# Optimization experiments

Hardware: AMD Instinct MI355X
Metric: run time of the kernel (lower is better)

The kernel has to match this reference:

```python
import jax, jax.numpy as jnp
import numpy as np

EPS = 1e-06

def _feature_map(x):
    # elu(x) + 1 -> strictly positive feature map
    return jax.nn.elu(x) + 1.0

def setup_inputs() -> dict:
    key = jax.random.key(0)
    kq, kk, kv = jax.random.split(key, 3)
    B, H, N, D = 1, 16, 2048, 64
    Q = jax.random.normal(kq, (B, H, N, D), dtype=jnp.float32)
    K = jax.random.normal(kk, (B, H, N, D), dtype=jnp.float32)
    V = jax.random.normal(kv, (B, H, N, D), dtype=jnp.float32)
    return {"Q": Q, "K": K, "V": V, "causal": 1}

def reference(Q, K, V, causal):
    Qf = _feature_map(Q)  # (B,H,N,D)
    Kf = _feature_map(K)  # (B,H,N,D)
    if causal:
        # prefix sums of per-position outer products K_m V_m^T  -> (B,H,N,D,Dv)
        KV_prefix = jnp.cumsum(Kf[..., :, None] * V[..., None, :], axis=2)
        Kf_prefix = jnp.cumsum(Kf, axis=2)  # (B,H,N,D)
        num = jnp.einsum('bhnd,bhnde->bhne', Qf, KV_prefix)
        den = jnp.einsum('bhnd,bhnd->bhn', Qf, Kf_prefix)[..., None]
        return num / (den + EPS)
    else:
        KV = jnp.einsum('bhnd,bhne->bhde', Kf, V)            # (B,H,D,Dv)
        num = jnp.einsum('bhnd,bhde->bhne', Qf, KV)          # (B,H,N,Dv)
        den = jnp.einsum('bhnd,bhd->bhn', Qf, Kf.sum(axis=2))[..., None]
        return num / (den + EPS)
```

## Files before the change

kernel.cpp:

```cpp
#include <hip/hip_runtime.h>

#define Hh   16
#define Nn   2048
#define Dd   64
#define DVv  64
#define Ll   64
#define Cc   (Nn / Ll)
#define HCc  (Hh * Cc)
#define EPSf 1e-6f
#define LDP  72

typedef __attribute__((ext_vector_type(8))) __bf16 bf16x8;
typedef __attribute__((ext_vector_type(4))) __bf16 bf16x4;
typedef __attribute__((ext_vector_type(4))) float  f32x4;

__device__ __forceinline__ float fmap(float x) {
    return x > 0.0f ? (x + 1.0f) : __expf(x);
}
__device__ __forceinline__ __bf16 tobf(float x) { return (__bf16)x; }

__global__ __launch_bounds__(256) void k_chunk_sums(
    const float* __restrict__ Kg, const float* __restrict__ Vg,
    __bf16* __restrict__ SwsT, float* __restrict__ zws)
{
    __shared__ __align__(16) __bf16 sKT[Dd][LDP];
    __shared__ __align__(16) __bf16 sVT[80][LDP];
    const int t  = threadIdx.x;
    const int hc = blockIdx.x;
    const float4* K4 = (const float4*)(Kg + (size_t)hc * (Ll * Dd));
    const float4* V4 = (const float4*)(Vg + (size_t)hc * (Ll * DVv));
    for (int i = t; i < (Ll * Dd) / 4; i += 256) {
        float4 k4 = K4[i];
        float4 v4 = V4[i];
        const int m  = i >> 4;
        const int c0 = (i & 15) * 4;
        sKT[c0 + 0][m] = tobf(fmap(k4.x));
        sKT[c0 + 1][m] = tobf(fmap(k4.y));
        sKT[c0 + 2][m] = tobf(fmap(k4.z));
        sKT[c0 + 3][m] = tobf(fmap(k4.w));
        sVT[c0 + 0][m] = tobf(v4.x);
        sVT[c0 + 1][m] = tobf(v4.y);
        sVT[c0 + 2][m] = tobf(v4.z);
        sVT[c0 + 3][m] = tobf(v4.w);
    }
    for (int i = t; i < 16 * LDP; i += 256) {
        const int r = i / LDP, c = i % LDP;
        sVT[64 + r][c] = (r == 0) ? (__bf16)1.0f : (__bf16)0.0f;
    }
    __syncthreads();

    const int lane = t & 63, wv = t >> 6;
    const int col = lane & 15, quad = lane >> 4;
    __bf16* So = SwsT + (size_t)hc * (Dd * DVv);
    for (int et = 0; et < 5; ++et) {
        f32x4 acc = {0.f, 0.f, 0.f, 0.f};
#pragma unroll
        for (int ks = 0; ks < 2; ++ks) {
            bf16x8 a = *(const bf16x8*)&sKT[wv * 16 + col][ks * 32 + quad * 8];
            bf16x8 b = *(const bf16x8*)&sVT[et * 16 + col][ks * 32 + quad * 8];
            acc = __builtin_amdgcn_mfma_f32_16x16x32_bf16(a, b, acc, 0, 0, 0);
        }
        if (et < 4) {
            const int e = et * 16 + col;
            const int d = wv * 16 + quad * 4;
            bf16x4 s4 = { tobf(acc[0]), tobf(acc[1]), tobf(acc[2]), tobf(acc[3]) };
            *(bf16x4*)&So[e * Dd + d] = s4;
        } else if (col == 0) {
#pragma unroll
            for (int j = 0; j < 4; ++j)
                zws[hc * Dd + wv * 16 + quad * 4 + j] = acc[j];
        }
    }
}

__global__ __launch_bounds__(256) void k_prefix(
    __bf16* __restrict__ SwsT, float* __restrict__ zws)
{
    const int b = blockIdx.x, t = threadIdx.x;
    if (b < 32) {
        const int gid = b * 256 + t;
        const int h   = gid >> 9;
        const int sl  = gid & 511;
        __bf16* base = SwsT + ((size_t)h * Cc) * (Dd * DVv) + sl * 8;
        float run[8];
#pragma unroll
        for (int j = 0; j < 8; ++j) run[j] = 0.0f;
#pragma unroll
        for (int cb = 0; cb < 4; ++cb) {
            bf16x8 v[8];
#pragma unroll
            for (int k = 0; k < 8; ++k)
                v[k] = *(const bf16x8*)(base + (size_t)(cb * 8 + k) * (Dd * DVv));
#pragma unroll
            for (int k = 0; k < 8; ++k) {
                bf16x8 o;
#pragma unroll
                for (int j = 0; j < 8; ++j) {
                    o[j] = tobf(run[j]);
                    run[j] += (float)v[k][j];
                }
                *(bf16x8*)(base + (size_t)(cb * 8 + k) * (Dd * DVv)) = o;
            }
        }
    } else {
        const int gid = (b - 32) * 256 + t;
        const int h = gid >> 6, d = gid & 63;
        float* zb = zws + (h * Cc) * Dd + d;
        float run = 0.0f;
#pragma unroll
        for (int cb = 0; cb < 4; ++cb) {
            float v[8];
#pragma unroll
            for (int k = 0; k < 8; ++k) v[k] = zb[(cb * 8 + k) * Dd];
#pragma unroll
            for (int k = 0; k < 8; ++k) {
                zb[(cb * 8 + k) * Dd] = run;
                run += v[k];
            }
        }
    }
}

__global__ __launch_bounds__(256) void k_output(
    const float* __restrict__ Qg, const float* __restrict__ Kg,
    const float* __restrict__ Vg, const __bf16* __restrict__ SwsT,
    const float* __restrict__ zws, float* __restrict__ Og)
{
    __shared__ __align__(16) __bf16 aQ[Ll][LDP];
    __shared__ __align__(16) __bf16 aK[Ll][LDP];
    __shared__ __align__(16) __bf16 sW[Ll][LDP];
    __shared__ __align__(16) __bf16 bV[80][LDP];
    __shared__ __align__(16) __bf16 bS[80][LDP];
    const int t  = threadIdx.x;
    const int hc = blockIdx.x;
    const int lane = t & 63, wv = t >> 6;
    const int col = lane & 15, quad = lane >> 4;

    {
        const float4* Q4 = (const float4*)(Qg + (size_t)hc * (Ll * Dd));
        const float4* K4 = (const float4*)(Kg + (size_t)hc * (Ll * Dd));
        const float4* V4 = (const float4*)(Vg + (size_t)hc * (Ll * DVv));
        for (int i = t; i < (Ll * Dd) / 4; i += 256) {
            float4 q4 = Q4[i];
            float4 k4 = K4[i];
            float4 v4 = V4[i];
            const int m  = i >> 4;
            const int c0 = (i & 15) * 4;
            bf16x4 qv = { tobf(fmap(q4.x)), tobf(fmap(q4.y)), tobf(fmap(q4.z)), tobf(fmap(q4.w)) };
            bf16x4 kv = { tobf(fmap(k4.x)), tobf(fmap(k4.y)), tobf(fmap(k4.z)), tobf(fmap(k4.w)) };
            *(bf16x4*)&aQ[m][c0] = qv;
            *(bf16x4*)&aK[m][c0] = kv;
            bV[c0 + 0][m] = tobf(v4.x);
            bV[c0 + 1][m] = tobf(v4.y);
            bV[c0 + 2][m] = tobf(v4.z);
            bV[c0 + 3][m] = tobf(v4.w);
        }
        for (int i = t; i < 16 * LDP; i += 256) {
            const int r = i / LDP, cc = i % LDP;
            bV[64 + r][cc] = (r == 0) ? (__bf16)1.0f : (__bf16)0.0f;
        }
    }

    {
        const __bf16* Sp = SwsT + (size_t)hc * (Dd * DVv);
        for (int i = t; i < (Dd * DVv) / 8; i += 256) {
            bf16x8 s = *(const bf16x8*)(Sp + i * 8);
            const int e = i >> 3, d0 = (i & 7) * 8;
            *(bf16x8*)&bS[e][d0] = s;
        }
        if (t < Dd) bS[64][t] = tobf(zws[hc * Dd + t]);
        for (int i = t; i < 16 * LDP; i += 256) {
            const int r = i / LDP, cc = i % LDP;
            if (!(r == 0 && cc < Dd)) bS[64 + r][cc] = (__bf16)0.0f;
        }
    }
    __syncthreads();

#pragma unroll 1
    for (int mt = 0; mt < 4; ++mt) {
        f32x4 wacc = {0.f, 0.f, 0.f, 0.f};
#pragma unroll
        for (int ks = 0; ks < 2; ++ks) {
            bf16x8 a = *(const bf16x8*)&aQ[wv * 16 + col][ks * 32 + quad * 8];
            bf16x8 b = *(const bf16x8*)&aK[mt * 16 + col][ks * 32 + quad * 8];
            wacc = __builtin_amdgcn_mfma_f32_16x16x32_bf16(a, b, wacc, 0, 0, 0);
        }
#pragma unroll
        for (int j = 0; j < 4; ++j) {
            const int n = wv * 16 + quad * 4 + j;
            const int m = mt * 16 + col;
            sW[n][m] = tobf(m <= n ? wacc[j] : 0.0f);
        }
    }
    __syncthreads();

    f32x4 accs[5];
#pragma unroll 1
    for (int et = 0; et < 5; ++et) {
        f32x4 acc = {0.f, 0.f, 0.f, 0.f};
#pragma unroll
        for (int ks = 0; ks < 2; ++ks) {
            bf16x8 a = *(const bf16x8*)&sW[wv * 16 + col][ks * 32 + quad * 8];
            bf16x8 b = *(const bf16x8*)&bV[et * 16 + col][ks * 32 + quad * 8];
            acc = __builtin_amdgcn_mfma_f32_16x16x32_bf16(a, b, acc, 0, 0, 0);
        }
#pragma unroll
        for (int ks = 0; ks < 2; ++ks) {
            bf16x8 a = *(const bf16x8*)&aQ[wv * 16 + col][ks * 32 + quad * 8];
            bf16x8 b = *(const bf16x8*)&bS[et * 16 + col][ks * 32 + quad * 8];
            acc = __builtin_amdgcn_mfma_f32_16x16x32_bf16(a, b, acc, 0, 0, 0);
        }
        accs[et] = acc;
    }
    float dn[4];
#pragma unroll
    for (int j = 0; j < 4; ++j) dn[j] = __shfl(accs[4][j], lane & 48);

    float* Oc = Og + (size_t)hc * (Ll * DVv);
#pragma unroll
    for (int et = 0; et < 4; ++et) {
#pragma unroll
        for (int j = 0; j < 4; ++j) {
            const int n = wv * 16 + quad * 4 + j;
            Oc[n * DVv + et * 16 + col] = accs[et][j] / (dn[j] + EPSf);
        }
    }
}

extern "C" void kernel_launch(void* const* d_in, const int* in_sizes, int n_in,
                              void* d_out, int out_size, void* d_ws, size_t ws_size,
                              hipStream_t stream) {
    const float* Q = (const float*)d_in[0];
    const float* K = (const float*)d_in[1];
    const float* V = (const float*)d_in[2];
    __bf16* SwsT = (__bf16*)d_ws;
    float*  zws  = (float*)((char*)d_ws + (size_t)HCc * Dd * DVv * sizeof(__bf16));
    float* out = (float*)d_out;

    k_chunk_sums<<<HCc, 256, 0, stream>>>(K, V, SwsT, zws);
    k_prefix<<<36, 256, 0, stream>>>(SwsT, zws);
    k_output<<<HCc, 256, 0, stream>>>(Q, K, V, SwsT, zws, out);
}
```

Before: 88.78 us.

## Fuse chunk-sum and prefix-scan kernels via last-block-per-head atomic counter

Merges the separate prefix-scan kernel into the chunk-sum kernel. The last block to finish for each head, found through an atomic counter, performs that head's prefix scan over the chunk state matrices and normaliser sums. This removes one kernel launch and its inter-kernel gap. In exchange it adds a memset on the same stream, threadfences, and serialised scan work on 16 blocks that each handle a whole head, so per-thread scan work is larger than in the old 36-block scan.

New measurement: 160.7 us. +81.0%, slower.

```diff
diff --git a/kernel.cpp b/kernel.cpp
--- a/kernel.cpp
+++ b/kernel.cpp
@@ -19,14 +19,17 @@
 }
 __device__ __forceinline__ __bf16 tobf(float x) { return (__bf16)x; }
 
-__global__ __launch_bounds__(256) void k_chunk_sums(
+__global__ __launch_bounds__(256) void k_chunk_scan(
     const float* __restrict__ Kg, const float* __restrict__ Vg,
-    __bf16* __restrict__ SwsT, float* __restrict__ zws)
+    __bf16* __restrict__ SwsT, float* __restrict__ zws,
+    unsigned int* __restrict__ cnt)
 {
     __shared__ __align__(16) __bf16 sKT[Dd][LDP];
     __shared__ __align__(16) __bf16 sVT[80][LDP];
+    __shared__ int isLast;
     const int t  = threadIdx.x;
     const int hc = blockIdx.x;
+    const int h  = hc >> 5;
     const float4* K4 = (const float4*)(Kg + (size_t)hc * (Ll * Dd));
     const float4* V4 = (const float4*)(Vg + (size_t)hc * (Ll * DVv));
     for (int i = t; i < (Ll * Dd) / 4; i += 256) {
@@ -71,51 +74,51 @@
                 zws[hc * Dd + wv * 16 + quad * 4 + j] = acc[j];
         }
     }
-}
-
-__global__ __launch_bounds__(256) void k_prefix(
-    __bf16* __restrict__ SwsT, float* __restrict__ zws)
-{
-    const int b = blockIdx.x, t = threadIdx.x;
-    if (b < 32) {
-        const int gid = b * 256 + t;
-        const int h   = gid >> 9;
-        const int sl  = gid & 511;
-        __bf16* base = SwsT + ((size_t)h * Cc) * (Dd * DVv) + sl * 8;
-        float run[8];
-#pragma unroll
-        for (int j = 0; j < 8; ++j) run[j] = 0.0f;
+
+    __threadfence();
+    __syncthreads();
+    if (t == 0) {
+        unsigned int old = atomicAdd(&cnt[h], 1u);
+        isLast = (old == (unsigned)(Cc - 1));
+    }
+    __syncthreads();
+    if (isLast) {
+        __threadfence();
+        __bf16* base = SwsT + ((size_t)h * Cc) * (Dd * DVv) + t * 16;
+        float run[16];
+#pragma unroll
+        for (int j = 0; j < 16; ++j) run[j] = 0.0f;
 #pragma unroll
         for (int cb = 0; cb < 4; ++cb) {
-            bf16x8 v[8];
-#pragma unroll
-            for (int k = 0; k < 8; ++k)
-                v[k] = *(const bf16x8*)(base + (size_t)(cb * 8 + k) * (Dd * DVv));
+            bf16x8 v0[8], v1[8];
 #pragma unroll
             for (int k = 0; k < 8; ++k) {
-                bf16x8 o;
-#pragma unroll
-                for (int j = 0; j < 8; ++j) {
-                    o[j] = tobf(run[j]);
-                    run[j] += (float)v[k][j];
-                }
-                *(bf16x8*)(base + (size_t)(cb * 8 + k) * (Dd * DVv)) = o;
+                const __bf16* p = base + (size_t)(cb * 8 + k) * (Dd * DVv);
+                v0[k] = *(const bf16x8*)p;
+                v1[k] = *(const bf16x8*)(p + 8);
             }
-        }
-    } else {
-        const int gid = (b - 32) * 256 + t;
-        const int h = gid >> 6, d = gid & 63;
-        float* zb = zws + (h * Cc) * Dd + d;
-        float run = 0.0f;
-#pragma unroll
-        for (int cb = 0; cb < 4; ++cb) {
-            float v[8];
-#pragma unroll
-            for (int k = 0; k < 8; ++k) v[k] = zb[(cb * 8 + k) * Dd];
 #pragma unroll
             for (int k = 0; k < 8; ++k) {
-                zb[(cb * 8 + k) * Dd] = run;
-                run += v[k];
+                __bf16* p = base + (size_t)(cb * 8 + k) * (Dd * DVv);
+                bf16x8 o0, o1;
+#pragma unroll
+                for (int j = 0; j < 8; ++j) { o0[j] = tobf(run[j]);     run[j]     += (float)v0[k][j]; }
+#pragma unroll
+                for (int j = 0; j < 8; ++j) { o1[j] = tobf(run[8 + j]); run[8 + j] += (float)v1[k][j]; }
+                *(bf16x8*)p       = o0;
+                *(bf16x8*)(p + 8) = o1;
+            }
+        }
+        if (t < Dd) {
+            float* zb = zws + (h * Cc) * Dd + t;
+            float zr = 0.0f;
+#pragma unroll
+            for (int cb = 0; cb < 4; ++cb) {
+                float v[8];
+#pragma unroll
+                for (int k = 0; k < 8; ++k) v[k] = zb[(cb * 8 + k) * Dd];
+#pragma unroll
+                for (int k = 0; k < 8; ++k) { zb[(cb * 8 + k) * Dd] = zr; zr += v[k]; }
             }
         }
     }
@@ -233,11 +236,15 @@
     const float* Q = (const float*)d_in[0];
     const float* K = (const float*)d_in[1];
     const float* V = (const float*)d_in[2];
-    __bf16* SwsT = (__bf16*)d_ws;
-    float*  zws  = (float*)((char*)d_ws + (size_t)HCc * Dd * DVv * sizeof(__bf16));
+    unsigned char* ws = (unsigned char*)d_ws;
+    const size_t s_bytes = (size_t)HCc * Dd * DVv * sizeof(__bf16);
+    const size_t z_bytes = (size_t)HCc * Dd * sizeof(float);
+    __bf16* SwsT = (__bf16*)ws;
+    float*  zws  = (float*)(ws + s_bytes);
+    unsigned int* cnt = (unsigned int*)(ws + s_bytes + z_bytes);
     float* out = (float*)d_out;
 
-    k_chunk_sums<<<HCc, 256, 0, stream>>>(K, V, SwsT, zws);
-    k_prefix<<<36, 256, 0, stream>>>(SwsT, zws);
+    hipMemsetAsync(cnt, 0, Hh * sizeof(unsigned int), stream);
+    k_chunk_scan<<<HCc, 256, 0, stream>>>(K, V, SwsT, zws, cnt);
     k_output<<<HCc, 256, 0, stream>>>(Q, K, V, SwsT, zws, out);
 }
```
